# Optimization experiments

Measured on AMD Instinct MI355X. Metric: run time of the kernel, lower is better.

Reference implementation:

```python
import jax, jax.numpy as jnp
import numpy as np

E = 768
H = 12
D = E // H  # 64


def setup_inputs() -> dict:
    key = jax.random.key(0)
    ks = jax.random.split(key, 12)
    B, S = 4, 2048
    scale = 1.0 / np.sqrt(E)
    inp = {
        "q": jax.random.normal(ks[0], (B, S, E), jnp.float32),
        "k": jax.random.normal(ks[1], (B, S, E), jnp.float32),
        "v": jax.random.normal(ks[2], (B, S, E), jnp.float32),
        "mask": jax.random.randint(ks[3], (B, S), 0, 2, jnp.int32),
        "Wq": jax.random.normal(ks[4], (E, E), jnp.float32) * scale,
        "bq": jnp.zeros((E,), jnp.float32),
        "Wk": jax.random.normal(ks[5], (E, E), jnp.float32) * scale,
        "bk": jnp.zeros((E,), jnp.float32),
        "Wv": jax.random.normal(ks[6], (E, E), jnp.float32) * scale,
        "bv": jnp.zeros((E,), jnp.float32),
        "Wo": jax.random.normal(ks[7], (E, E), jnp.float32) * scale,
        "bo": jnp.zeros((E,), jnp.float32),
    }
    return inp


def reference(q, k, v, mask, Wq, bq, Wk, bk, Wv, bv, Wo, bo):
    B, Sq, _ = q.shape
    Sk = k.shape[1]
    # QKV projections, split into heads: [B, H, S, D]
    qh = (q @ Wq + bq).reshape(B, Sq, H, D).transpose(0, 2, 1, 3)
    kh = (k @ Wk + bk).reshape(B, Sk, H, D).transpose(0, 2, 1, 3)
    vh = (v @ Wv + bv).reshape(B, Sk, H, D).transpose(0, 2, 1, 3)
    scores = jnp.einsum("bhqd,bhkd->bhqk", qh, kh) / jnp.sqrt(jnp.float32(D))
    # enc=True padding-mask path: positions where mask==0 get -1e9 added
    bias = jnp.where(mask == 0, jnp.float32(-1e9), jnp.float32(0.0))  # [B, Sk]
    scores = scores + bias[:, None, None, :]
    weights = jax.nn.softmax(scores, axis=-1)
    # dropout is identity in eval mode
    ctx = jnp.einsum("bhqk,bhkd->bqhd", weights, vh).reshape(B, Sq, E)
    return ctx @ Wo + bo
```

## Files before the change

kernel.cpp:

```cpp
#include <hip/hip_runtime.h>
#include <hip/hip_bf16.h>
#include <stdint.h>


typedef __bf16 bf16x8 __attribute__((ext_vector_type(8)));
typedef __bf16 bf16x4 __attribute__((ext_vector_type(4)));
typedef float floatx4 __attribute__((ext_vector_type(4)));

#define MFMA_BF16(a, b, c) __builtin_amdgcn_mfma_f32_16x16x32_bf16(a, b, c, 0, 0, 0)


__device__ __forceinline__ void glds16(const __bf16* g, __bf16* l) {
  __builtin_amdgcn_global_load_lds(
      (const __attribute__((address_space(1))) unsigned int*)g,
      (__attribute__((address_space(3))) unsigned int*)l, 16, 0, 0);
}

__global__ __launch_bounds__(256) void prep_convert(
    const float* __restrict__ q, const float* __restrict__ k,
    const float* __restrict__ v, __bf16* __restrict__ Xq,
    __bf16* __restrict__ Xk, __bf16* __restrict__ Xv) {
  const int z = blockIdx.y;
  const float* src = (z == 0) ? q : (z == 1) ? k : v;
  __bf16* dst = (z == 0) ? Xq : (z == 1) ? Xk : Xv;
  const size_t i8 = ((size_t)blockIdx.x * 256 + threadIdx.x) * 8;
  float4 f0 = *(const float4*)&src[i8];
  float4 f1 = *(const float4*)&src[i8 + 4];
  bf16x8 o;
  o[0] = (__bf16)f0.x; o[1] = (__bf16)f0.y; o[2] = (__bf16)f0.z; o[3] = (__bf16)f0.w;
  o[4] = (__bf16)f1.x; o[5] = (__bf16)f1.y; o[6] = (__bf16)f1.z; o[7] = (__bf16)f1.w;
  *(bf16x8*)&dst[i8] = o;
}

__global__ __launch_bounds__(256) void prep_transpose(
    const float* __restrict__ W0, const float* __restrict__ W1,
    const float* __restrict__ W2, const float* __restrict__ W3,
    __bf16* __restrict__ T0, __bf16* __restrict__ T1,
    __bf16* __restrict__ T2, __bf16* __restrict__ T3) {
  const int z = blockIdx.z;
  const float* W = (z == 0) ? W0 : (z == 1) ? W1 : (z == 2) ? W2 : W3;
  __bf16* T = (z == 0) ? T0 : (z == 1) ? T1 : (z == 2) ? T2 : T3;
  __shared__ float t[32][33];
  const int tx = threadIdx.x & 31, ty = threadIdx.x >> 5;
  const int kb = blockIdx.x * 32, nb = blockIdx.y * 32;
#pragma unroll
  for (int j = 0; j < 4; ++j)
    t[ty + j * 8][tx] = W[(size_t)(kb + ty + j * 8) * 768 + nb + tx];
  __syncthreads();
#pragma unroll
  for (int j = 0; j < 4; ++j)
    T[(size_t)(nb + ty + j * 8) * 768 + kb + tx] = (__bf16)t[tx][ty + j * 8];
}

__global__ __launch_bounds__(256) void qkv_gemm(
    const __bf16* __restrict__ Wtq, const __bf16* __restrict__ Wtk,
    const __bf16* __restrict__ Wtv, const __bf16* __restrict__ Xq,
    const __bf16* __restrict__ Xk, const __bf16* __restrict__ Xv,
    const float* __restrict__ bq, const float* __restrict__ bk,
    const float* __restrict__ bv, __bf16* __restrict__ Qh,
    __bf16* __restrict__ Kh, __bf16* __restrict__ Vt) {
  __shared__ __align__(16) __bf16 As[128 * 32];
  __shared__ __align__(16) __bf16 Bs[128 * 32];
  const int z = blockIdx.z;
  const __bf16* Aop = (z == 0) ? Wtq : (z == 1) ? Wtk : Wtv;
  const __bf16* Bop = (z == 0) ? Xq : (z == 1) ? Xk : Xv;
  const float* bias = (z == 0) ? bq : (z == 1) ? bk : bv;
  __bf16* Dst = (z == 0) ? Qh : (z == 1) ? Kh : Vt;
  const int m0 = blockIdx.x * 128, n0 = blockIdx.y * 128;

  const int tid = threadIdx.x, lane = tid & 63, w = tid >> 6;
  const int quad = lane >> 4, l16 = lane & 15;
  const int wm = (w >> 1) * 64, wn = (w & 1) * 64;

  const int grow = w * 32 + (lane >> 2);
  const int gcol = (lane & 3) * 8;
  const __bf16* gA = Aop + (size_t)(m0 + grow) * 768 + gcol;
  const __bf16* gB = Bop + (size_t)(n0 + grow) * 768 + gcol;
  __bf16* lA = As + w * 1024;
  __bf16* lB = Bs + w * 1024;

  floatx4 acc[4][4] = {};

  for (int k0 = 0; k0 < 768; k0 += 32) {
    __syncthreads();
    glds16(gA, lA);
    glds16(gA + (size_t)16 * 768, lA + 512);
    glds16(gB, lB);
    glds16(gB + (size_t)16 * 768, lB + 512);
    gA += 32;
    gB += 32;
    __syncthreads();
    bf16x8 af[4], bfr[4];
#pragma unroll
    for (int t = 0; t < 4; ++t) {
      af[t] = *(const bf16x8*)&As[(wm + t * 16 + l16) * 32 + quad * 8];
      bfr[t] = *(const bf16x8*)&Bs[(wn + t * 16 + l16) * 32 + quad * 8];
    }
#pragma unroll
    for (int mt = 0; mt < 4; ++mt)
#pragma unroll
      for (int nt = 0; nt < 4; ++nt)
        acc[mt][nt] = MFMA_BF16(af[mt], bfr[nt], acc[mt][nt]);
  }

#pragma unroll
  for (int mt = 0; mt < 4; ++mt) {
    const int e = m0 + wm + mt * 16 + quad * 4;
    const float4 b4 = *(const float4*)&bias[e];
    const int h = e >> 6, d = e & 63;
#pragma unroll
    for (int nt = 0; nt < 4; ++nt) {
      const int s = n0 + wn + nt * 16 + l16;
      const int bb = s >> 11, sr = s & 2047;
      const float v0 = acc[mt][nt][0] + b4.x;
      const float v1 = acc[mt][nt][1] + b4.y;
      const float v2 = acc[mt][nt][2] + b4.z;
      const float v3 = acc[mt][nt][3] + b4.w;
      if (z < 2) {
        bf16x4 pv;
        pv[0] = (__bf16)v0; pv[1] = (__bf16)v1; pv[2] = (__bf16)v2; pv[3] = (__bf16)v3;
        const int col = (z == 0) ? d : ((((d >> 3) ^ (sr & 7)) << 3) | (d & 7));
        *(bf16x4*)&Dst[((size_t)(bb * 12 + h) * 2048 + sr) * 64 + col] = pv;
      } else {
        const size_t rowbase = ((size_t)(bb * 12 + h) * 64 + d) * 2048;
        const int shi = sr & ~63, sblk = (sr >> 3) & 7, soff = sr & 7;
        Dst[rowbase + 0 * 2048 + shi + (((sblk ^ ((d + 0) & 7))) << 3) + soff] = (__bf16)v0;
        Dst[rowbase + 1 * 2048 + shi + (((sblk ^ ((d + 1) & 7))) << 3) + soff] = (__bf16)v1;
        Dst[rowbase + 2 * 2048 + shi + (((sblk ^ ((d + 2) & 7))) << 3) + soff] = (__bf16)v2;
        Dst[rowbase + 3 * 2048 + shi + (((sblk ^ ((d + 3) & 7))) << 3) + soff] = (__bf16)v3;
      }
    }
  }
}

__global__ __launch_bounds__(256) void out_gemm(const __bf16* __restrict__ Wto,
                                                const __bf16* __restrict__ Ctx,
                                                const float* __restrict__ bo,
                                                float* __restrict__ Out) {
  __shared__ __align__(16) __bf16 As[128 * 32];
  __shared__ __align__(16) __bf16 Bs[128 * 32];
  const int m0 = blockIdx.x * 128, n0 = blockIdx.y * 128;
  const int tid = threadIdx.x, lane = tid & 63, w = tid >> 6;
  const int quad = lane >> 4, l16 = lane & 15;
  const int wm = (w >> 1) * 64, wn = (w & 1) * 64;

  const int grow = w * 32 + (lane >> 2);
  const int gcol = (lane & 3) * 8;
  const __bf16* gA = Wto + (size_t)(m0 + grow) * 768 + gcol;
  const __bf16* gB = Ctx + (size_t)(n0 + grow) * 768 + gcol;
  __bf16* lA = As + w * 1024;
  __bf16* lB = Bs + w * 1024;

  floatx4 acc[4][4] = {};
  for (int k0 = 0; k0 < 768; k0 += 32) {
    __syncthreads();
    glds16(gA, lA);
    glds16(gA + (size_t)16 * 768, lA + 512);
    glds16(gB, lB);
    glds16(gB + (size_t)16 * 768, lB + 512);
    gA += 32;
    gB += 32;
    __syncthreads();
    bf16x8 af[4], bfr[4];
#pragma unroll
    for (int t = 0; t < 4; ++t) {
      af[t] = *(const bf16x8*)&As[(wm + t * 16 + l16) * 32 + quad * 8];
      bfr[t] = *(const bf16x8*)&Bs[(wn + t * 16 + l16) * 32 + quad * 8];
    }
#pragma unroll
    for (int mt = 0; mt < 4; ++mt)
#pragma unroll
      for (int nt = 0; nt < 4; ++nt)
        acc[mt][nt] = MFMA_BF16(af[mt], bfr[nt], acc[mt][nt]);
  }

#pragma unroll
  for (int mt = 0; mt < 4; ++mt) {
    const int e = m0 + wm + mt * 16 + quad * 4;
    const float4 b4 = *(const float4*)&bo[e];
#pragma unroll
    for (int nt = 0; nt < 4; ++nt) {
      const int s = n0 + wn + nt * 16 + l16;
      float4 r;
      r.x = acc[mt][nt][0] + b4.x;
      r.y = acc[mt][nt][1] + b4.y;
      r.z = acc[mt][nt][2] + b4.z;
      r.w = acc[mt][nt][3] + b4.w;
      *(float4*)&Out[(size_t)s * 768 + e] = r;
    }
  }
}

__global__ __launch_bounds__(256) void attn_kernel(
    const __bf16* __restrict__ Qh, const __bf16* __restrict__ Kh,
    const __bf16* __restrict__ Vt, const int* __restrict__ mask,
    __bf16* __restrict__ ctx) {
  const int bh = blockIdx.y, b = bh / 12, h = bh - b * 12;
  const int tid = threadIdx.x, lane = tid & 63, w = tid >> 6;
  const int quad = lane >> 4, l16 = lane & 15;
  const int q0 = blockIdx.x * 128 + w * 32;

  __shared__ float biasS[2048];
  __shared__ __align__(16) __bf16 Ks[64 * 64];
  __shared__ __align__(16) __bf16 Vs[64 * 64];
  __shared__ __align__(16) __bf16 Plds[4][32][72];

  for (int i = tid; i < 2048; i += 256)
    biasS[i] = mask[b * 2048 + i] ? 0.0f : -1e5f;
  __syncthreads();

  const __bf16* Qbase = Qh + (size_t)bh * 2048 * 64;
  const __bf16* Kbase = Kh + (size_t)bh * 2048 * 64;
  const __bf16* Vbase = Vt + (size_t)bh * 64 * 2048;

  bf16x8 bqf[2][2];
#pragma unroll
  for (int qt = 0; qt < 2; ++qt)
#pragma unroll
    for (int c = 0; c < 2; ++c)
      bqf[qt][c] =
          *(const bf16x8*)&Qbase[(size_t)(q0 + qt * 16 + l16) * 64 + c * 32 + quad * 8];

  const int srow = (lane >> 3);
  const int scol = (lane & 7) * 8;
  const int col0 = (quad ^ (l16 & 7)) * 8;

  floatx4 o[4][2] = {};
  float rS[2] = {0.0f, 0.0f};
  const float SC = 0.18033688011112042f;

  for (int kt = 0; kt < 2048; kt += 64) {
    __syncthreads();
#pragma unroll
    for (int j = 0; j < 2; ++j) {
      const int c = w * 2 + j;
      const int row = c * 8 + srow;
      glds16(&Kbase[(size_t)(kt + row) * 64 + scol], Ks + c * 512);
      glds16(&Vbase[(size_t)row * 2048 + kt + scol], Vs + c * 512);
    }
    __syncthreads();

    floatx4 sc[4][2];
#pragma unroll
    for (int t = 0; t < 4; ++t) {
      bf16x8 ak0 = *(const bf16x8*)&Ks[(t * 16 + l16) * 64 + col0];
      bf16x8 ak1 = *(const bf16x8*)&Ks[(t * 16 + l16) * 64 + (col0 ^ 32)];
#pragma unroll
      for (int qt = 0; qt < 2; ++qt) {
        floatx4 zz = {};
        zz = MFMA_BF16(ak0, bqf[qt][0], zz);
        zz = MFMA_BF16(ak1, bqf[qt][1], zz);
        sc[t][qt] = zz;
      }
    }
#pragma unroll
    for (int t = 0; t < 4; ++t) {
      const float4 kb = *(const float4*)&biasS[kt + t * 16 + quad * 4];
#pragma unroll
      for (int qt = 0; qt < 2; ++qt) {
        floatx4 p;
        p[0] = exp2f(fmaf(sc[t][qt][0], SC, kb.x));
        p[1] = exp2f(fmaf(sc[t][qt][1], SC, kb.y));
        p[2] = exp2f(fmaf(sc[t][qt][2], SC, kb.z));
        p[3] = exp2f(fmaf(sc[t][qt][3], SC, kb.w));
        sc[t][qt] = p;
        rS[qt] += p[0] + p[1] + p[2] + p[3];
      }
    }
#pragma unroll
    for (int qt = 0; qt < 2; ++qt)
#pragma unroll
      for (int t = 0; t < 4; ++t) {
        bf16x4 pv;
        pv[0] = (__bf16)sc[t][qt][0];
        pv[1] = (__bf16)sc[t][qt][1];
        pv[2] = (__bf16)sc[t][qt][2];
        pv[3] = (__bf16)sc[t][qt][3];
        *(bf16x4*)&Plds[w][qt * 16 + l16][t * 16 + quad * 4] = pv;
      }
#pragma unroll
    for (int c = 0; c < 2; ++c) {
      bf16x8 bp[2];
#pragma unroll
      for (int qt = 0; qt < 2; ++qt)
        bp[qt] = *(const bf16x8*)&Plds[w][qt * 16 + l16][c * 32 + quad * 8];
#pragma unroll
      for (int dt = 0; dt < 4; ++dt) {
        bf16x8 av = *(const bf16x8*)&Vs[(dt * 16 + l16) * 64 + (col0 ^ (c * 32))];
#pragma unroll
        for (int qt = 0; qt < 2; ++qt) o[dt][qt] = MFMA_BF16(av, bp[qt], o[dt][qt]);
      }
    }
  }

  float inv[2];
#pragma unroll
  for (int qt = 0; qt < 2; ++qt) {
    float s = rS[qt];
    s += __shfl_xor(s, 16, 64);
    s += __shfl_xor(s, 32, 64);
    inv[qt] = 1.0f / s;
  }
#pragma unroll
  for (int dt = 0; dt < 4; ++dt)
#pragma unroll
    for (int qt = 0; qt < 2; ++qt) {
      const int q = q0 + qt * 16 + l16;
      const int d = h * 64 + dt * 16 + quad * 4;
      bf16x4 pv;
      pv[0] = (__bf16)(o[dt][qt][0] * inv[qt]);
      pv[1] = (__bf16)(o[dt][qt][1] * inv[qt]);
      pv[2] = (__bf16)(o[dt][qt][2] * inv[qt]);
      pv[3] = (__bf16)(o[dt][qt][3] * inv[qt]);
      *(bf16x4*)&ctx[(size_t)(b * 2048 + q) * 768 + d] = pv;
    }
}

extern "C" void kernel_launch(void* const* d_in, const int* in_sizes, int n_in,
                              void* d_out, int out_size, void* d_ws, size_t ws_size,
                              hipStream_t stream) {
  const float* q = (const float*)d_in[0];
  const float* k = (const float*)d_in[1];
  const float* v = (const float*)d_in[2];
  const int* mask = (const int*)d_in[3];
  const float* Wq = (const float*)d_in[4];
  const float* bq = (const float*)d_in[5];
  const float* Wk = (const float*)d_in[6];
  const float* bk = (const float*)d_in[7];
  const float* Wv = (const float*)d_in[8];
  const float* bv = (const float*)d_in[9];
  const float* Wo = (const float*)d_in[10];
  const float* bo = (const float*)d_in[11];
  float* out = (float*)d_out;

  char* ws = (char*)d_ws;
  const size_t SZ = (size_t)8192 * 768 * 2;
  const size_t WSZ = (size_t)768 * 768 * 2;
  __bf16* Xq = (__bf16*)(ws);
  __bf16* Xk = (__bf16*)(ws + SZ);
  __bf16* Xv = (__bf16*)(ws + 2 * SZ);
  __bf16* Qh = (__bf16*)(ws + 3 * SZ);
  __bf16* Kh = (__bf16*)(ws + 4 * SZ);
  __bf16* Vt = (__bf16*)(ws + 5 * SZ);
  __bf16* ctx = (__bf16*)(ws + 6 * SZ);
  __bf16* Wtq = (__bf16*)(ws + 7 * SZ);
  __bf16* Wtk = (__bf16*)(ws + 7 * SZ + WSZ);
  __bf16* Wtv = (__bf16*)(ws + 7 * SZ + 2 * WSZ);
  __bf16* Wto = (__bf16*)(ws + 7 * SZ + 3 * WSZ);

  prep_convert<<<dim3(3072, 3), 256, 0, stream>>>(q, k, v, Xq, Xk, Xv);
  prep_transpose<<<dim3(24, 24, 4), 256, 0, stream>>>(Wq, Wk, Wv, Wo, Wtq, Wtk, Wtv, Wto);
  qkv_gemm<<<dim3(6, 64, 3), 256, 0, stream>>>(Wtq, Wtk, Wtv, Xq, Xk, Xv, bq, bk, bv,
                                               Qh, Kh, Vt);
  attn_kernel<<<dim3(16, 48), 256, 0, stream>>>(Qh, Kh, Vt, mask, ctx);
  out_gemm<<<dim3(6, 64), 256, 0, stream>>>(Wto, ctx, bo, out);
}
```

Measured before the change: 320.2 us.

## Double-buffer attention K/V tiles, vectorize V projection stores, shrink output GEMM tiles

```diff
diff --git a/kernel.cpp b/kernel.cpp
--- a/kernel.cpp
+++ b/kernel.cpp
@@ -62,11 +62,10 @@
   __shared__ __align__(16) __bf16 As[128 * 32];
   __shared__ __align__(16) __bf16 Bs[128 * 32];
   const int z = blockIdx.z;
-  const __bf16* Aop = (z == 0) ? Wtq : (z == 1) ? Wtk : Wtv;
-  const __bf16* Bop = (z == 0) ? Xq : (z == 1) ? Xk : Xv;
-  const float* bias = (z == 0) ? bq : (z == 1) ? bk : bv;
-  __bf16* Dst = (z == 0) ? Qh : (z == 1) ? Kh : Vt;
-  const int m0 = blockIdx.x * 128, n0 = blockIdx.y * 128;
+  const __bf16* Aop = (z == 0) ? Wtq : (z == 1) ? Wtk : Xv;
+  const __bf16* Bop = (z == 0) ? Xq : (z == 1) ? Xk : Wtv;
+  const int m0 = ((z == 2) ? blockIdx.y : blockIdx.x) * 128;
+  const int n0 = ((z == 2) ? blockIdx.x : blockIdx.y) * 128;
 
   const int tid = threadIdx.x, lane = tid & 63, w = tid >> 6;
   const int quad = lane >> 4, l16 = lane & 15;
@@ -103,31 +102,48 @@
         acc[mt][nt] = MFMA_BF16(af[mt], bfr[nt], acc[mt][nt]);
   }
 
-#pragma unroll
-  for (int mt = 0; mt < 4; ++mt) {
-    const int e = m0 + wm + mt * 16 + quad * 4;
-    const float4 b4 = *(const float4*)&bias[e];
-    const int h = e >> 6, d = e & 63;
-#pragma unroll
-    for (int nt = 0; nt < 4; ++nt) {
-      const int s = n0 + wn + nt * 16 + l16;
-      const int bb = s >> 11, sr = s & 2047;
-      const float v0 = acc[mt][nt][0] + b4.x;
-      const float v1 = acc[mt][nt][1] + b4.y;
-      const float v2 = acc[mt][nt][2] + b4.z;
-      const float v3 = acc[mt][nt][3] + b4.w;
-      if (z < 2) {
+  if (z < 2) {
+    const float* bias = (z == 0) ? bq : bk;
+    __bf16* Dst = (z == 0) ? Qh : Kh;
+#pragma unroll
+    for (int mt = 0; mt < 4; ++mt) {
+      const int e = m0 + wm + mt * 16 + quad * 4;
+      const float4 b4 = *(const float4*)&bias[e];
+      const int h = e >> 6, d = e & 63;
+#pragma unroll
+      for (int nt = 0; nt < 4; ++nt) {
+        const int s = n0 + wn + nt * 16 + l16;
+        const int bb = s >> 11, sr = s & 2047;
         bf16x4 pv;
-        pv[0] = (__bf16)v0; pv[1] = (__bf16)v1; pv[2] = (__bf16)v2; pv[3] = (__bf16)v3;
+        pv[0] = (__bf16)(acc[mt][nt][0] + b4.x);
+        pv[1] = (__bf16)(acc[mt][nt][1] + b4.y);
+        pv[2] = (__bf16)(acc[mt][nt][2] + b4.z);
+        pv[3] = (__bf16)(acc[mt][nt][3] + b4.w);
         const int col = (z == 0) ? d : ((((d >> 3) ^ (sr & 7)) << 3) | (d & 7));
         *(bf16x4*)&Dst[((size_t)(bb * 12 + h) * 2048 + sr) * 64 + col] = pv;
-      } else {
-        const size_t rowbase = ((size_t)(bb * 12 + h) * 64 + d) * 2048;
-        const int shi = sr & ~63, sblk = (sr >> 3) & 7, soff = sr & 7;
-        Dst[rowbase + 0 * 2048 + shi + (((sblk ^ ((d + 0) & 7))) << 3) + soff] = (__bf16)v0;
-        Dst[rowbase + 1 * 2048 + shi + (((sblk ^ ((d + 1) & 7))) << 3) + soff] = (__bf16)v1;
-        Dst[rowbase + 2 * 2048 + shi + (((sblk ^ ((d + 2) & 7))) << 3) + soff] = (__bf16)v2;
-        Dst[rowbase + 3 * 2048 + shi + (((sblk ^ ((d + 3) & 7))) << 3) + soff] = (__bf16)v3;
+      }
+    }
+  } else {
+    float bvn[4];
+#pragma unroll
+    for (int nt = 0; nt < 4; ++nt) bvn[nt] = bv[n0 + wn + nt * 16 + l16];
+#pragma unroll
+    for (int mt = 0; mt < 4; ++mt) {
+      const int s = m0 + wm + mt * 16 + quad * 4;
+      const int bb = s >> 11, sr = s & 2047;
+      const int shi = sr & ~63, sblk = (sr >> 3) & 7, soff = sr & 7;
+#pragma unroll
+      for (int nt = 0; nt < 4; ++nt) {
+        const int e = n0 + wn + nt * 16 + l16;
+        const int h = e >> 6, d = e & 63;
+        bf16x4 pv;
+        pv[0] = (__bf16)(acc[mt][nt][0] + bvn[nt]);
+        pv[1] = (__bf16)(acc[mt][nt][1] + bvn[nt]);
+        pv[2] = (__bf16)(acc[mt][nt][2] + bvn[nt]);
+        pv[3] = (__bf16)(acc[mt][nt][3] + bvn[nt]);
+        const size_t addr = ((size_t)(bb * 12 + h) * 64 + d) * 2048 + shi +
+                            ((sblk ^ (d & 7)) << 3) + soff;
+        *(bf16x4*)&Vt[addr] = pv;
       }
     }
   }
@@ -137,45 +153,44 @@
                                                 const __bf16* __restrict__ Ctx,
                                                 const float* __restrict__ bo,
                                                 float* __restrict__ Out) {
-  __shared__ __align__(16) __bf16 As[128 * 32];
+  __shared__ __align__(16) __bf16 As[64 * 32];
   __shared__ __align__(16) __bf16 Bs[128 * 32];
-  const int m0 = blockIdx.x * 128, n0 = blockIdx.y * 128;
+  const int m0 = blockIdx.x * 64, n0 = blockIdx.y * 128;
   const int tid = threadIdx.x, lane = tid & 63, w = tid >> 6;
   const int quad = lane >> 4, l16 = lane & 15;
-  const int wm = (w >> 1) * 64, wn = (w & 1) * 64;
-
-  const int grow = w * 32 + (lane >> 2);
+  const int wm = (w >> 1) * 32, wn = (w & 1) * 64;
+
   const int gcol = (lane & 3) * 8;
-  const __bf16* gA = Wto + (size_t)(m0 + grow) * 768 + gcol;
-  const __bf16* gB = Ctx + (size_t)(n0 + grow) * 768 + gcol;
-  __bf16* lA = As + w * 1024;
+  const __bf16* gA = Wto + (size_t)(m0 + w * 16 + (lane >> 2)) * 768 + gcol;
+  const __bf16* gB = Ctx + (size_t)(n0 + w * 32 + (lane >> 2)) * 768 + gcol;
+  __bf16* lA = As + w * 512;
   __bf16* lB = Bs + w * 1024;
 
-  floatx4 acc[4][4] = {};
+  floatx4 acc[2][4] = {};
   for (int k0 = 0; k0 < 768; k0 += 32) {
     __syncthreads();
     glds16(gA, lA);
-    glds16(gA + (size_t)16 * 768, lA + 512);
     glds16(gB, lB);
     glds16(gB + (size_t)16 * 768, lB + 512);
     gA += 32;
     gB += 32;
     __syncthreads();
-    bf16x8 af[4], bfr[4];
-#pragma unroll
-    for (int t = 0; t < 4; ++t) {
+    bf16x8 af[2], bfr[4];
+#pragma unroll
+    for (int t = 0; t < 2; ++t)
       af[t] = *(const bf16x8*)&As[(wm + t * 16 + l16) * 32 + quad * 8];
+#pragma unroll
+    for (int t = 0; t < 4; ++t)
       bfr[t] = *(const bf16x8*)&Bs[(wn + t * 16 + l16) * 32 + quad * 8];
-    }
-#pragma unroll
-    for (int mt = 0; mt < 4; ++mt)
+#pragma unroll
+    for (int mt = 0; mt < 2; ++mt)
 #pragma unroll
       for (int nt = 0; nt < 4; ++nt)
         acc[mt][nt] = MFMA_BF16(af[mt], bfr[nt], acc[mt][nt]);
   }
 
 #pragma unroll
-  for (int mt = 0; mt < 4; ++mt) {
+  for (int mt = 0; mt < 2; ++mt) {
     const int e = m0 + wm + mt * 16 + quad * 4;
     const float4 b4 = *(const float4*)&bo[e];
 #pragma unroll
@@ -200,14 +215,9 @@
   const int quad = lane >> 4, l16 = lane & 15;
   const int q0 = blockIdx.x * 128 + w * 32;
 
-  __shared__ float biasS[2048];
-  __shared__ __align__(16) __bf16 Ks[64 * 64];
-  __shared__ __align__(16) __bf16 Vs[64 * 64];
+  __shared__ __align__(16) __bf16 Ks[2][64 * 64];
+  __shared__ __align__(16) __bf16 Vs[2][64 * 64];
   __shared__ __align__(16) __bf16 Plds[4][32][72];
-
-  for (int i = tid; i < 2048; i += 256)
-    biasS[i] = mask[b * 2048 + i] ? 0.0f : -1e5f;
-  __syncthreads();
 
   const __bf16* Qbase = Qh + (size_t)bh * 2048 * 64;
   const __bf16* Kbase = Kh + (size_t)bh * 2048 * 64;
@@ -221,30 +231,46 @@
       bqf[qt][c] =
           *(const bf16x8*)&Qbase[(size_t)(q0 + qt * 16 + l16) * 64 + c * 32 + quad * 8];
 
-  const int srow = (lane >> 3);
+  const int r0 = w * 16 + (lane >> 3);
   const int scol = (lane & 7) * 8;
+  const int ldsOff = w * 1024;
+  const __bf16* pK = Kbase + (size_t)r0 * 64 + scol;
+  const __bf16* pV = Vbase + (size_t)r0 * 2048 + scol;
+  const int* pM = mask + b * 2048 + quad * 4;
   const int col0 = (quad ^ (l16 & 7)) * 8;
+
+  glds16(pK, &Ks[0][ldsOff]);
+  glds16(pK + 512, &Ks[0][ldsOff + 512]);
+  glds16(pV, &Vs[0][ldsOff]);
+  glds16(pV + 16384, &Vs[0][ldsOff + 512]);
+  pK += 4096;
+  pV += 64;
 
   floatx4 o[4][2] = {};
   float rS[2] = {0.0f, 0.0f};
   const float SC = 0.18033688011112042f;
 
-  for (int kt = 0; kt < 2048; kt += 64) {
-    __syncthreads();
-#pragma unroll
-    for (int j = 0; j < 2; ++j) {
-      const int c = w * 2 + j;
-      const int row = c * 8 + srow;
-      glds16(&Kbase[(size_t)(kt + row) * 64 + scol], Ks + c * 512);
-      glds16(&Vbase[(size_t)row * 2048 + kt + scol], Vs + c * 512);
-    }
-    __syncthreads();
+  auto body = [&](int cur) {
+    const int nxt = cur ^ 1;
+    __syncthreads();
+
+    glds16(pK, &Ks[nxt][ldsOff]);
+    glds16(pK + 512, &Ks[nxt][ldsOff + 512]);
+    glds16(pV, &Vs[nxt][ldsOff]);
+    glds16(pV + 16384, &Vs[nxt][ldsOff + 512]);
+    pK += 4096;
+    pV += 64;
+
+    int4 mk[4];
+#pragma unroll
+    for (int t = 0; t < 4; ++t) mk[t] = *(const int4*)(pM + t * 16);
+    pM += 64;
 
     floatx4 sc[4][2];
 #pragma unroll
     for (int t = 0; t < 4; ++t) {
-      bf16x8 ak0 = *(const bf16x8*)&Ks[(t * 16 + l16) * 64 + col0];
-      bf16x8 ak1 = *(const bf16x8*)&Ks[(t * 16 + l16) * 64 + (col0 ^ 32)];
+      bf16x8 ak0 = *(const bf16x8*)&Ks[cur][(t * 16 + l16) * 64 + col0];
+      bf16x8 ak1 = *(const bf16x8*)&Ks[cur][(t * 16 + l16) * 64 + (col0 ^ 32)];
 #pragma unroll
       for (int qt = 0; qt < 2; ++qt) {
         floatx4 zz = {};
@@ -255,14 +281,17 @@
     }
 #pragma unroll
     for (int t = 0; t < 4; ++t) {
-      const float4 kb = *(const float4*)&biasS[kt + t * 16 + quad * 4];
+      const float k0f = mk[t].x ? 0.0f : -1e5f;
+      const float k1f = mk[t].y ? 0.0f : -1e5f;
+      const float k2f = mk[t].z ? 0.0f : -1e5f;
+      const float k3f = mk[t].w ? 0.0f : -1e5f;
 #pragma unroll
       for (int qt = 0; qt < 2; ++qt) {
         floatx4 p;
-        p[0] = exp2f(fmaf(sc[t][qt][0], SC, kb.x));
-        p[1] = exp2f(fmaf(sc[t][qt][1], SC, kb.y));
-        p[2] = exp2f(fmaf(sc[t][qt][2], SC, kb.z));
-        p[3] = exp2f(fmaf(sc[t][qt][3], SC, kb.w));
+        p[0] = __builtin_amdgcn_exp2f(fmaf(sc[t][qt][0], SC, k0f));
+        p[1] = __builtin_amdgcn_exp2f(fmaf(sc[t][qt][1], SC, k1f));
+        p[2] = __builtin_amdgcn_exp2f(fmaf(sc[t][qt][2], SC, k2f));
+        p[3] = __builtin_amdgcn_exp2f(fmaf(sc[t][qt][3], SC, k3f));
         sc[t][qt] = p;
         rS[qt] += p[0] + p[1] + p[2] + p[3];
       }
@@ -286,11 +315,16 @@
         bp[qt] = *(const bf16x8*)&Plds[w][qt * 16 + l16][c * 32 + quad * 8];
 #pragma unroll
       for (int dt = 0; dt < 4; ++dt) {
-        bf16x8 av = *(const bf16x8*)&Vs[(dt * 16 + l16) * 64 + (col0 ^ (c * 32))];
+        bf16x8 av = *(const bf16x8*)&Vs[cur][(dt * 16 + l16) * 64 + (col0 ^ (c * 32))];
 #pragma unroll
         for (int qt = 0; qt < 2; ++qt) o[dt][qt] = MFMA_BF16(av, bp[qt], o[dt][qt]);
       }
     }
+  };
+
+  for (int it = 0; it < 16; ++it) {
+    body(0);
+    body(1);
   }
 
   float inv[2];
@@ -353,5 +387,5 @@
   qkv_gemm<<<dim3(6, 64, 3), 256, 0, stream>>>(Wtq, Wtk, Wtv, Xq, Xk, Xv, bq, bk, bv,
                                                Qh, Kh, Vt);
   attn_kernel<<<dim3(16, 48), 256, 0, stream>>>(Qh, Kh, Vt, mask, ctx);
-  out_gemm<<<dim3(6, 64), 256, 0, stream>>>(Wto, ctx, bo, out);
-}
+  out_gemm<<<dim3(12, 64), 256, 0, stream>>>(Wto, ctx, bo, out);
+}
```

New measurement: 324.9 us. No clear change (+1.5%).
